# Kernel tuning notes

Measured on AMD Instinct MI355X. Metric: run time of the kernel, lower is better.

The kernel has to match this reference:

```python
import jax, jax.numpy as jnp
import numpy as np

B, S, IN, OUT, RANK, NLANG = 4, 4096, 1024, 4096, 32, 9


def setup_inputs() -> dict:
    key = jax.random.key(0)
    k_x, k_w, k_w1 = jax.random.split(key, 3)
    x = jax.random.normal(k_x, (B, S, IN), dtype=jnp.float32)
    # base Linear weight (xavier-uniform in torch; gaussian fine for a numeric baseline)
    weight = jax.random.normal(k_w, (OUT, IN), dtype=jnp.float32) * 0.02
    bias = jnp.zeros((OUT,), dtype=jnp.float32)
    # per-language low-rank factors; torch inits w1 ~ N(0, 0.01), w2 zeros --
    # use small random values for both so gradients/outputs are non-trivial
    w1 = jax.random.normal(k_w1, (NLANG, OUT, RANK), dtype=jnp.float32) * 0.01
    w2 = jax.random.normal(jax.random.fold_in(key, 7), (NLANG, RANK, IN), dtype=jnp.float32) * 0.01
    return {"x": x, "weight": weight, "bias": bias, "w1": w1, "w2": w2,
            "src_id": 0, "tgt_id": 3}


def reference(x, weight, bias, w1, w2, src_id, tgt_id):
    # pair LMS delta: full [OUT, IN] low-rank matrix, as in the torch module
    delta = w1[src_id] @ w2[tgt_id]          # [OUT, RANK] @ [RANK, IN] -> [OUT, IN]
    w_eff = weight + delta
    # F.linear: x @ W^T + b
    return jnp.einsum('bsi,oi->bso', x, w_eff) + bias
```

## Files before the change

kernel.cpp:

```cpp
#include <hip/hip_runtime.h>

#define B_DIM 4
#define S_DIM 4096
#define IN_DIM 1024
#define OUT_DIM 4096
#define RANK_DIM 32

#define M_DIM (B_DIM * S_DIM)
#define N_DIM OUT_DIM
#define K_DIM IN_DIM

#define CVT_BLOCKS ((M_DIM * K_DIM) / 1024)

typedef _Float16 h4 __attribute__((ext_vector_type(4)));
typedef _Float16 h8 __attribute__((ext_vector_type(8)));
typedef float f32x16 __attribute__((ext_vector_type(16)));

__device__ __forceinline__ void async_load16(const void* g, void* l) {
  __builtin_amdgcn_global_load_lds((const __attribute__((address_space(1))) void*)g,
                                   (__attribute__((address_space(3))) void*)l,
                                   16, 0, 0);
}

__global__ __launch_bounds__(256) void prep_fused_kernel(
    const float4* __restrict__ x, h4* __restrict__ xh,
    const float* __restrict__ weight, const float* __restrict__ w1,
    const float* __restrict__ w2, const int* __restrict__ src_id,
    const int* __restrict__ tgt_id, h4* __restrict__ weff) {
  if (blockIdx.x < CVT_BLOCKS) {
    const int i = blockIdx.x * 256 + threadIdx.x;
    const float4 v = x[i];
    h4 o;
    o[0] = (_Float16)v.x; o[1] = (_Float16)v.y;
    o[2] = (_Float16)v.z; o[3] = (_Float16)v.w;
    xh[i] = o;
  } else {
    const int n = blockIdx.x - CVT_BLOCKS;
    const int src = src_id[0];
    const int tgt = tgt_id[0];
    __shared__ float w1r[RANK_DIM];
    if (threadIdx.x < RANK_DIM)
      w1r[threadIdx.x] = w1[((size_t)src * OUT_DIM + n) * RANK_DIM + threadIdx.x];
    __syncthreads();
    const int k4 = threadIdx.x;
    float4 acc = ((const float4*)(weight + (size_t)n * IN_DIM))[k4];
    const float* w2t = w2 + (size_t)tgt * RANK_DIM * IN_DIM;
#pragma unroll 8
    for (int r = 0; r < RANK_DIM; ++r) {
      const float4 wv = ((const float4*)(w2t + (size_t)r * IN_DIM))[k4];
      const float c = w1r[r];
      acc.x += c * wv.x; acc.y += c * wv.y; acc.z += c * wv.z; acc.w += c * wv.w;
    }
    h4 o;
    o[0] = (_Float16)acc.x; o[1] = (_Float16)acc.y;
    o[2] = (_Float16)acc.z; o[3] = (_Float16)acc.w;
    weff[(size_t)n * (IN_DIM / 4) + k4] = o;
  }
}

__global__ __launch_bounds__(512, 2) void lms_gemm256_kernel(
    const _Float16* __restrict__ A,
    const _Float16* __restrict__ Bt,
    const float* __restrict__ bias,
    float* __restrict__ C) {
  __shared__ _Float16 sA[4][8192];
  __shared__ _Float16 sB[4][8192];

  const int tid = threadIdx.x;
  const int wave = tid >> 6;
  const int lane = tid & 63;

  const int bid = blockIdx.x;
  const int wg = (bid & 7) * 128 + (bid >> 3);
  const int bm = wg >> 4;
  const int bn = wg & 15;

  const int wr = wave >> 2;
  const int wc = wave & 3;
  const int fr = lane & 31;
  const int kq = lane >> 5;
  const int key = (fr >> 1) & 3;
  const int aBase = (wr * 128 + fr) * 32;
  const int bBase = (wc * 64 + fr) * 32;
  const int bo0 = (kq ^ key) << 3;
  const int bo1 = bo0 ^ 16;

  const int srow = wave * 16 + (lane >> 2);
  const int sblk = (lane & 3) ^ ((lane >> 3) & 3);
  const _Float16* gA = A + (size_t)(bm * 256 + srow) * K_DIM + sblk * 8;
  const _Float16* gB = Bt + (size_t)(bn * 256 + srow) * K_DIM + sblk * 8;

  f32x16 acc[4][2] = {};

#define STAGE_TILE(nA, nB, KOFF)                                              \
  {                                                                           \
    async_load16(gA + (KOFF), (nA) + wave * 512);                             \
    async_load16(gA + (KOFF) + 128 * K_DIM, (nA) + 4096 + wave * 512);        \
    async_load16(gB + (KOFF), (nB) + wave * 512);                             \
    async_load16(gB + (KOFF) + 128 * K_DIM, (nB) + 4096 + wave * 512);        \
  }

#define KBODY(cA, cB, nA, nB, DO_STAGE, KOFF, WAITBAR)                        \
  {                                                                           \
    if (DO_STAGE) STAGE_TILE(nA, nB, KOFF);                                   \
    h8 af[4][2], bf[2][2];                                                    \
    _Pragma("unroll") for (int mi = 0; mi < 4; ++mi) {                        \
      af[mi][0] = *(const h8*)&(cA)[aBase + mi * 1024 + bo0];                 \
      af[mi][1] = *(const h8*)&(cA)[aBase + mi * 1024 + bo1];                 \
    }                                                                         \
    _Pragma("unroll") for (int ni = 0; ni < 2; ++ni) {                        \
      bf[ni][0] = *(const h8*)&(cB)[bBase + ni * 1024 + bo0];                 \
      bf[ni][1] = *(const h8*)&(cB)[bBase + ni * 1024 + bo1];                 \
    }                                                                         \
    __builtin_amdgcn_s_setprio(1);                                            \
    _Pragma("unroll") for (int ks = 0; ks < 2; ++ks)                          \
      _Pragma("unroll") for (int mi = 0; mi < 4; ++mi)                        \
        _Pragma("unroll") for (int ni = 0; ni < 2; ++ni)                      \
          acc[mi][ni] = __builtin_amdgcn_mfma_f32_32x32x16_f16(               \
              af[mi][ks], bf[ni][ks], acc[mi][ni], 0, 0, 0);                  \
    __builtin_amdgcn_s_setprio(0);                                            \
    WAITBAR;                                                                  \
  }

#define WB8 asm volatile("s_waitcnt vmcnt(8) lgkmcnt(0)\ns_barrier" ::: "memory")
#define WB4 asm volatile("s_waitcnt vmcnt(4) lgkmcnt(0)\ns_barrier" ::: "memory")
#define WB0 asm volatile("s_waitcnt vmcnt(0) lgkmcnt(0)\ns_barrier" ::: "memory")

  STAGE_TILE(sA[0], sB[0], 0);
  STAGE_TILE(sA[1], sB[1], 32);
  STAGE_TILE(sA[2], sB[2], 64);
  asm volatile("s_waitcnt vmcnt(8)\ns_barrier" ::: "memory");

  for (int t = 0; t < 28; t += 4) {
    const int ko = t * 32;
    KBODY(sA[0], sB[0], sA[3], sB[3], true, ko + 96,  WB8);
    KBODY(sA[1], sB[1], sA[0], sB[0], true, ko + 128, WB8);
    KBODY(sA[2], sB[2], sA[1], sB[1], true, ko + 160, WB8);
    KBODY(sA[3], sB[3], sA[2], sB[2], true, ko + 192, WB8);
  }
  KBODY(sA[0], sB[0], sA[3], sB[3], true, 31 * 32, WB8);
  KBODY(sA[1], sB[1], sA[0], sB[0], false, 0, WB4);
  KBODY(sA[2], sB[2], sA[1], sB[1], false, 0, WB0);
  KBODY(sA[3], sB[3], sA[2], sB[2], false, 0, (void)0);

  const int cn = fr;
  const int rq = (lane >> 5) * 4;
#pragma unroll
  for (int ni = 0; ni < 2; ++ni) {
    const int col = bn * 256 + wc * 64 + ni * 32 + cn;
    const float bv = bias[col];
#pragma unroll
    for (int mi = 0; mi < 4; ++mi) {
      const int rowb = bm * 256 + wr * 128 + mi * 32 + rq;
      float* cp = C + (size_t)rowb * N_DIM + col;
#pragma unroll
      for (int reg = 0; reg < 16; ++reg) {
        const int roff = (reg & 3) + 8 * (reg >> 2);
        cp[(size_t)roff * N_DIM] = acc[mi][ni][reg] + bv;
      }
    }
  }
}

extern "C" void kernel_launch(void* const* d_in, const int* in_sizes, int n_in,
                              void* d_out, int out_size, void* d_ws, size_t ws_size,
                              hipStream_t stream) {
  const float* x      = (const float*)d_in[0];
  const float* weight = (const float*)d_in[1];
  const float* bias   = (const float*)d_in[2];
  const float* w1     = (const float*)d_in[3];
  const float* w2     = (const float*)d_in[4];
  const int* src_id   = (const int*)d_in[5];
  const int* tgt_id   = (const int*)d_in[6];
  float* out          = (float*)d_out;

  _Float16* xh   = (_Float16*)d_ws;
  _Float16* weff = xh + (size_t)M_DIM * K_DIM;

  prep_fused_kernel<<<CVT_BLOCKS + N_DIM, 256, 0, stream>>>(
      (const float4*)x, (h4*)xh, weight, w1, w2, src_id, tgt_id, (h4*)weff);

  lms_gemm256_kernel<<<dim3(1024), dim3(512), 0, stream>>>(xh, weff, bias, out);
}
```

Baseline: 485.4 us.

## Restructure GEMM mainloop into 8-phase ping-pong with 16x16x32 MFMA

Replaces the 4-stage k32 LDS ring with a double-buffered k64 scheme split into two k32 halves. Each k-half is processed in two M-half phases, with barriers around every phase and global-to-LDS staging interleaved per phase. It also switches from 32x32x16 to 16x16x32 MFMA with 8x4 accumulator tiles and drops the XOR swizzle on LDS addressing. The aim is finer-grained overlap of loads with MFMA work, at the cost of more barriers and possible LDS bank conflicts from the unswizzled layout.

```diff
diff --git a/kernel.cpp b/kernel.cpp
--- a/kernel.cpp
+++ b/kernel.cpp
@@ -14,7 +14,7 @@
 
 typedef _Float16 h4 __attribute__((ext_vector_type(4)));
 typedef _Float16 h8 __attribute__((ext_vector_type(8)));
-typedef float f32x16 __attribute__((ext_vector_type(16)));
+typedef float f32x4 __attribute__((ext_vector_type(4)));
 
 __device__ __forceinline__ void async_load16(const void* g, void* l) {
   __builtin_amdgcn_global_load_lds((const __attribute__((address_space(1))) void*)g,
@@ -63,8 +63,8 @@
     const _Float16* __restrict__ Bt,
     const float* __restrict__ bias,
     float* __restrict__ C) {
-  __shared__ _Float16 sA[4][8192];
-  __shared__ _Float16 sB[4][8192];
+  __shared__ _Float16 sA[2][2][8192];
+  __shared__ _Float16 sB[2][2][8192];
 
   const int tid = threadIdx.x;
   const int wave = tid >> 6;
@@ -77,86 +77,95 @@
 
   const int wr = wave >> 2;
   const int wc = wave & 3;
-  const int fr = lane & 31;
-  const int kq = lane >> 5;
-  const int key = (fr >> 1) & 3;
-  const int aBase = (wr * 128 + fr) * 32;
-  const int bBase = (wc * 64 + fr) * 32;
-  const int bo0 = (kq ^ key) << 3;
-  const int bo1 = bo0 ^ 16;
+  const int fl = lane & 15;
+  const int ch = lane >> 4;
 
-  const int srow = wave * 16 + (lane >> 2);
-  const int sblk = (lane & 3) ^ ((lane >> 3) & 3);
-  const _Float16* gA = A + (size_t)(bm * 256 + srow) * K_DIM + sblk * 8;
-  const _Float16* gB = Bt + (size_t)(bn * 256 + srow) * K_DIM + sblk * 8;
+  const _Float16* gA = A + (size_t)(bm * 256 + (tid >> 2)) * K_DIM + (tid & 3) * 8;
+  const _Float16* gB = Bt + (size_t)(bn * 256 + (tid >> 2)) * K_DIM + (tid & 3) * 8;
 
-  f32x16 acc[4][2] = {};
+  f32x4 acc[8][4] = {};
+  h8 bf[4];
 
-#define STAGE_TILE(nA, nB, KOFF)                                              \
+#define STG_A(NB, KH, KN)                                                     \
   {                                                                           \
-    async_load16(gA + (KOFF), (nA) + wave * 512);                             \
-    async_load16(gA + (KOFF) + 128 * K_DIM, (nA) + 4096 + wave * 512);        \
-    async_load16(gB + (KOFF), (nB) + wave * 512);                             \
-    async_load16(gB + (KOFF) + 128 * K_DIM, (nB) + 4096 + wave * 512);        \
+    async_load16(gA + (KN) + (KH) * 32, &sA[NB][KH][wave * 512]);             \
+    async_load16(gA + (KN) + (KH) * 32 + (size_t)128 * K_DIM,                 \
+                 &sA[NB][KH][4096 + wave * 512]);                             \
+  }
+#define STG_B(NB, KH, KN)                                                     \
+  {                                                                           \
+    async_load16(gB + (KN) + (KH) * 32, &sB[NB][KH][wave * 512]);             \
+    async_load16(gB + (KN) + (KH) * 32 + (size_t)128 * K_DIM,                 \
+                 &sB[NB][KH][4096 + wave * 512]);                             \
+  }
+#define VM4 asm volatile("s_waitcnt vmcnt(4)" ::: "memory")
+#define VM0 asm volatile("s_waitcnt vmcnt(0)" ::: "memory")
+#define VM_NONE
+#define NOSTG
+
+#define PHASE(CB, KH, MH, STAGE_STMT, TRAIL)                                  \
+  {                                                                           \
+    h8 af[4];                                                                 \
+    _Pragma("unroll") for (int mi = 0; mi < 4; ++mi)                          \
+      af[mi] = *(const h8*)&sA[CB][KH]                                        \
+          [(wr * 128 + (MH) * 64 + mi * 16 + fl) * 32 + ch * 8];              \
+    if ((MH) == 0) {                                                          \
+      _Pragma("unroll") for (int ni = 0; ni < 4; ++ni)                        \
+        bf[ni] = *(const h8*)&sB[CB][KH]                                      \
+            [(wc * 64 + ni * 16 + fl) * 32 + ch * 8];                         \
+    }                                                                         \
+    STAGE_STMT;                                                               \
+    __builtin_amdgcn_s_barrier();                                             \
+    __builtin_amdgcn_s_setprio(1);                                            \
+    _Pragma("unroll") for (int mi = 0; mi < 4; ++mi)                          \
+      _Pragma("unroll") for (int ni = 0; ni < 4; ++ni)                        \
+        acc[(MH) * 4 + mi][ni] = __builtin_amdgcn_mfma_f32_16x16x32_f16(      \
+            af[mi], bf[ni], acc[(MH) * 4 + mi][ni], 0, 0, 0);                 \
+    __builtin_amdgcn_s_setprio(0);                                            \
+    TRAIL;                                                                    \
+    __builtin_amdgcn_s_barrier();                                             \
   }
 
-#define KBODY(cA, cB, nA, nB, DO_STAGE, KOFF, WAITBAR)                        \
-  {                                                                           \
-    if (DO_STAGE) STAGE_TILE(nA, nB, KOFF);                                   \
-    h8 af[4][2], bf[2][2];                                                    \
-    _Pragma("unroll") for (int mi = 0; mi < 4; ++mi) {                        \
-      af[mi][0] = *(const h8*)&(cA)[aBase + mi * 1024 + bo0];                 \
-      af[mi][1] = *(const h8*)&(cA)[aBase + mi * 1024 + bo1];                 \
-    }                                                                         \
-    _Pragma("unroll") for (int ni = 0; ni < 2; ++ni) {                        \
-      bf[ni][0] = *(const h8*)&(cB)[bBase + ni * 1024 + bo0];                 \
-      bf[ni][1] = *(const h8*)&(cB)[bBase + ni * 1024 + bo1];                 \
-    }                                                                         \
-    __builtin_amdgcn_s_setprio(1);                                            \
-    _Pragma("unroll") for (int ks = 0; ks < 2; ++ks)                          \
-      _Pragma("unroll") for (int mi = 0; mi < 4; ++mi)                        \
-        _Pragma("unroll") for (int ni = 0; ni < 2; ++ni)                      \
-          acc[mi][ni] = __builtin_amdgcn_mfma_f32_32x32x16_f16(               \
-              af[mi][ks], bf[ni][ks], acc[mi][ni], 0, 0, 0);                  \
-    __builtin_amdgcn_s_setprio(0);                                            \
-    WAITBAR;                                                                  \
+  STG_A(0, 0, 0);
+  STG_B(0, 0, 0);
+  STG_A(0, 1, 0);
+  STG_B(0, 1, 0);
+  asm volatile("s_waitcnt vmcnt(4)" ::: "memory");
+  __builtin_amdgcn_s_barrier();
+
+#pragma unroll 1
+  for (int it = 0; it < 7; ++it) {
+    const int kn0 = it * 128 + 64;
+    const int kn1 = kn0 + 64;
+    PHASE(0, 0, 0, STG_A(1, 0, kn0), VM_NONE);
+    PHASE(0, 0, 1, STG_B(1, 0, kn0), VM4);
+    PHASE(0, 1, 0, STG_A(1, 1, kn0), VM_NONE);
+    PHASE(0, 1, 1, STG_B(1, 1, kn0), VM4);
+    PHASE(1, 0, 0, STG_A(0, 0, kn1), VM_NONE);
+    PHASE(1, 0, 1, STG_B(0, 0, kn1), VM4);
+    PHASE(1, 1, 0, STG_A(0, 1, kn1), VM_NONE);
+    PHASE(1, 1, 1, STG_B(0, 1, kn1), VM4);
   }
+  PHASE(0, 0, 0, STG_A(1, 0, 960), VM_NONE);
+  PHASE(0, 0, 1, STG_B(1, 0, 960), VM4);
+  PHASE(0, 1, 0, STG_A(1, 1, 960), VM_NONE);
+  PHASE(0, 1, 1, STG_B(1, 1, 960), VM4);
+  PHASE(1, 0, 0, NOSTG, VM_NONE);
+  PHASE(1, 0, 1, NOSTG, VM0);
+  PHASE(1, 1, 0, NOSTG, VM_NONE);
+  PHASE(1, 1, 1, NOSTG, VM_NONE);
 
-#define WB8 asm volatile("s_waitcnt vmcnt(8) lgkmcnt(0)\ns_barrier" ::: "memory")
-#define WB4 asm volatile("s_waitcnt vmcnt(4) lgkmcnt(0)\ns_barrier" ::: "memory")
-#define WB0 asm volatile("s_waitcnt vmcnt(0) lgkmcnt(0)\ns_barrier" ::: "memory")
-
-  STAGE_TILE(sA[0], sB[0], 0);
-  STAGE_TILE(sA[1], sB[1], 32);
-  STAGE_TILE(sA[2], sB[2], 64);
-  asm volatile("s_waitcnt vmcnt(8)\ns_barrier" ::: "memory");
-
-  for (int t = 0; t < 28; t += 4) {
-    const int ko = t * 32;
-    KBODY(sA[0], sB[0], sA[3], sB[3], true, ko + 96,  WB8);
-    KBODY(sA[1], sB[1], sA[0], sB[0], true, ko + 128, WB8);
-    KBODY(sA[2], sB[2], sA[1], sB[1], true, ko + 160, WB8);
-    KBODY(sA[3], sB[3], sA[2], sB[2], true, ko + 192, WB8);
-  }
-  KBODY(sA[0], sB[0], sA[3], sB[3], true, 31 * 32, WB8);
-  KBODY(sA[1], sB[1], sA[0], sB[0], false, 0, WB4);
-  KBODY(sA[2], sB[2], sA[1], sB[1], false, 0, WB0);
-  KBODY(sA[3], sB[3], sA[2], sB[2], false, 0, (void)0);
-
-  const int cn = fr;
-  const int rq = (lane >> 5) * 4;
 #pragma unroll
-  for (int ni = 0; ni < 2; ++ni) {
-    const int col = bn * 256 + wc * 64 + ni * 32 + cn;
+  for (int ni = 0; ni < 4; ++ni) {
+    const int col = bn * 256 + wc * 64 + ni * 16 + fl;
     const float bv = bias[col];
 #pragma unroll
-    for (int mi = 0; mi < 4; ++mi) {
-      const int rowb = bm * 256 + wr * 128 + mi * 32 + rq;
+    for (int mi = 0; mi < 8; ++mi) {
+      const int rowb = bm * 256 + wr * 128 + mi * 16 + ch * 4;
       float* cp = C + (size_t)rowb * N_DIM + col;
 #pragma unroll
-      for (int reg = 0; reg < 16; ++reg) {
-        const int roff = (reg & 3) + 8 * (reg >> 2);
-        cp[(size_t)roff * N_DIM] = acc[mi][ni][reg] + bv;
+      for (int r = 0; r < 4; ++r) {
+        cp[(size_t)r * N_DIM] = acc[mi][ni][r] + bv;
       }
     }
   }
```

Result: slower. 508.7 us (+4.8%).
